# Kernel optimization log

Hardware: AMD Instinct MI355X
Metric: run time of the kernel (lower is better)

## Reference

```python
import jax, jax.numpy as jnp
import numpy as np

VOCAB = 100000
EMB = 256
HID = 512
H2 = HID // 2
TAGS = 6
START = 3
STOP = 4
NEG = -10000.0
T = 4096


def setup_inputs() -> dict:
    key = jax.random.key(0)
    ks = jax.random.split(key, 16)
    s = 0.05
    trans = jax.random.normal(ks[12], (TAGS, TAGS), dtype=jnp.float32)
    trans = trans.at[START, :].set(NEG).at[:, STOP].set(NEG)
    return {
        "sentence": jax.random.randint(ks[0], (T,), 0, VOCAB, dtype=jnp.int32),
        "emb": jax.random.normal(ks[1], (VOCAB, EMB), dtype=jnp.float32) * s,
        "w_ih_f": jax.random.normal(ks[2], (4 * H2, EMB), dtype=jnp.float32) * s,
        "w_hh_f": jax.random.normal(ks[3], (4 * H2, H2), dtype=jnp.float32) * s,
        "b_ih_f": jax.random.normal(ks[4], (4 * H2,), dtype=jnp.float32) * s,
        "b_hh_f": jax.random.normal(ks[5], (4 * H2,), dtype=jnp.float32) * s,
        "w_ih_b": jax.random.normal(ks[6], (4 * H2, EMB), dtype=jnp.float32) * s,
        "w_hh_b": jax.random.normal(ks[7], (4 * H2, H2), dtype=jnp.float32) * s,
        "b_ih_b": jax.random.normal(ks[8], (4 * H2,), dtype=jnp.float32) * s,
        "b_hh_b": jax.random.normal(ks[9], (4 * H2,), dtype=jnp.float32) * s,
        "W_out": jax.random.normal(ks[10], (TAGS, HID), dtype=jnp.float32) * s,
        "b_out": jax.random.normal(ks[11], (TAGS,), dtype=jnp.float32) * s,
        "transitions": trans,
        "h0": jax.random.normal(ks[13], (2, H2), dtype=jnp.float32),
        "c0": jax.random.normal(ks[14], (2, H2), dtype=jnp.float32),
    }


def _lstm_dir(x, h0, c0, w_ih, w_hh, b_ih, b_hh, reverse):
    # x: (T, E); PyTorch LSTM gate order i, f, g, o
    def step(carry, xt):
        h, c = carry
        z = xt @ w_ih.T + b_ih + h @ w_hh.T + b_hh
        i, f, g, o = jnp.split(z, 4)
        i = jax.nn.sigmoid(i)
        f = jax.nn.sigmoid(f)
        g = jnp.tanh(g)
        o = jax.nn.sigmoid(o)
        c = f * c + i * g
        h = o * jnp.tanh(c)
        return (h, c), h

    _, hs = jax.lax.scan(step, (h0, c0), x, reverse=reverse)
    return hs  # (T, H2), time-aligned for both directions


def reference(sentence, emb, w_ih_f, w_hh_f, b_ih_f, b_hh_f,
              w_ih_b, w_hh_b, b_ih_b, b_hh_b, W_out, b_out,
              transitions, h0, c0):
    x = emb[sentence]  # (T, E)
    hf = _lstm_dir(x, h0[0], c0[0], w_ih_f, w_hh_f, b_ih_f, b_hh_f, False)
    hb = _lstm_dir(x, h0[1], c0[1], w_ih_b, w_hh_b, b_ih_b, b_hh_b, True)
    feats = jnp.concatenate([hf, hb], axis=-1) @ W_out.T + b_out  # (T, TAGS)

    init = jnp.full((TAGS,), NEG, dtype=feats.dtype).at[START].set(0.0)

    def vstep(fv, feat):
        tmp = transitions + fv[None, :]          # (to, from)
        bp = jnp.argmax(tmp, axis=1)             # best prev tag per next tag
        fv_new = tmp[jnp.arange(TAGS), bp] + feat
        return fv_new, bp

    fv, bptrs = jax.lax.scan(vstep, init, feats)  # bptrs: (T, TAGS)
    term = fv + transitions[STOP]
    best = jnp.argmax(term)
    score = term[best]

    def btstep(tag, bp):
        return bp[tag], tag

    _, path = jax.lax.scan(btstep, best, bptrs, reverse=True)  # (T,)
    return score, path
```

## Files before the change

### kernel.cpp

```cpp
#include <hip/hip_runtime.h>
#include <stdint.h>
#include <math.h>

#define T 4096
#define NTAGS 6
#define START_TAG 3
#define STOP_TAG 4
#define NEGV -10000.0f
#define FLAG_MAGIC 0x5A000000u

__global__ __launch_bounds__(256) void k0_prep(
    const float* __restrict__ wf, const float* __restrict__ wb,
    const float* __restrict__ bif, const float* __restrict__ bhf,
    const float* __restrict__ bib, const float* __restrict__ bhb,
    float* __restrict__ wT, float* __restrict__ bias2) {
  int idx = blockIdx.x * 256 + threadIdx.x;
  int k = idx >> 11, col = idx & 2047;
  int d = col >> 10, g = col & 1023;
  const float* w = d ? wb : wf;
  wT[idx] = w[g * 256 + k];
  if (idx < 2048) bias2[idx] = d ? (bib[g] + bhb[g]) : (bif[g] + bhf[g]);
}

__global__ __launch_bounds__(256) void k1_zpre(
    const int* __restrict__ sent, const float* __restrict__ emb,
    const float* __restrict__ wT, const float* __restrict__ bias2,
    float* __restrict__ zpre) {
  int tb = blockIdx.x, cb = blockIdx.y;
  int tid = threadIdx.x;
  int col = cb * 256 + tid;
  int d = col >> 10, g = col & 1023;
  __shared__ float xs[32 * 256];
  int t0 = tb * 32;
  for (int r = 0; r < 32; r++) {
    int s = sent[t0 + r];
    xs[r * 256 + tid] = emb[(size_t)s * 256 + tid];
  }
  __syncthreads();
  float acc[32];
#pragma unroll
  for (int r = 0; r < 32; r++) acc[r] = 0.f;
  const float4* xs4 = (const float4*)xs;
  for (int kq = 0; kq < 64; kq++) {
    float w0 = wT[(4 * kq + 0) * 2048 + col];
    float w1 = wT[(4 * kq + 1) * 2048 + col];
    float w2 = wT[(4 * kq + 2) * 2048 + col];
    float w3 = wT[(4 * kq + 3) * 2048 + col];
#pragma unroll
    for (int r = 0; r < 32; r++) {
      float4 x4 = xs4[r * 64 + kq];
      acc[r] += w0 * x4.x + w1 * x4.y + w2 * x4.z + w3 * x4.w;
    }
  }
  float bb = bias2[col];
  for (int r = 0; r < 32; r++)
    zpre[((size_t)d * T + (t0 + r)) * 1024 + g] = acc[r] + bb;
}

__global__ __launch_bounds__(1024) void k2_lstm(
    const float* __restrict__ zpre,
    const float* __restrict__ whf, const float* __restrict__ whb,
    const float* __restrict__ h0, const float* __restrict__ c0,
    float* h_all, unsigned int* flags) {
  int bx = blockIdx.x;
  int d = bx >> 2, wg = bx & 3;
  const float* w_hh = d ? whb : whf;
  int tid = threadIdx.x;
  int row = tid >> 2, q = tid & 3;
  int gate = row >> 6, cl = row & 63;
  int B = wg * 64;
  int g_row = gate * 256 + B + cl;

  float4 w4[16];
  {
    const float4* wp = (const float4*)(w_hh + (size_t)g_row * 256 + q * 64);
#pragma unroll
    for (int m = 0; m < 16; m++) w4[m] = wp[m];
  }
  __shared__ float h_pad[4 * 72];
  __shared__ float z_lds[256];
  __shared__ float zin[256];
  float c = 0.f;
  if (tid < 64) c = c0[d * 256 + B + tid];
  const float* zp_d = zpre + (size_t)d * T * 1024;
  float* h_d = h_all + (size_t)d * T * 256;
  unsigned int* flg = flags + d * T * 4;

  for (int s = 0; s < T; s++) {
    int t = d ? (T - 1 - s) : s;
    float zv = 0.f;
    if (tid < 256) {
      int lg = tid >> 6, lc = tid & 63;
      zv = zp_d[(size_t)t * 1024 + lg * 256 + B + lc];
    }
    if (s == 0) {
      if (tid < 256) h_pad[(tid >> 6) * 72 + (tid & 63)] = h0[d * 256 + tid];
    } else {
      if (tid < 4) {
        unsigned int expv = FLAG_MAGIC + (unsigned)(s - 1);
        while (__hip_atomic_load(&flg[(s - 1) * 4 + tid], __ATOMIC_RELAXED,
                                 __HIP_MEMORY_SCOPE_AGENT) != expv) { }
      }
      __syncthreads();
      if (tid < 256) {
        int tprev = d ? (t + 1) : (t - 1);
        float hv = __hip_atomic_load(&h_d[(size_t)tprev * 256 + tid],
                                     __ATOMIC_RELAXED, __HIP_MEMORY_SCOPE_AGENT);
        h_pad[(tid >> 6) * 72 + (tid & 63)] = hv;
      }
    }
    if (tid < 256) zin[tid] = zv;
    __syncthreads();

    const float4* hp = (const float4*)(h_pad + q * 72);
    float acc = 0.f;
#pragma unroll
    for (int m = 0; m < 16; m++) {
      float4 h4 = hp[m];
      acc += w4[m].x * h4.x;
      acc += w4[m].y * h4.y;
      acc += w4[m].z * h4.z;
      acc += w4[m].w * h4.w;
    }
    acc += __shfl_xor(acc, 1);
    acc += __shfl_xor(acc, 2);
    if (q == 0) {
      float z = acc + zin[row];
      float a = (gate == 2) ? tanhf(z) : 1.f / (1.f + expf(-z));
      z_lds[row] = a;
    }
    __syncthreads();
    if (tid < 64) {
      float iA = z_lds[tid], fA = z_lds[64 + tid];
      float gA = z_lds[128 + tid], oA = z_lds[192 + tid];
      c = fA * c + iA * gA;
      float hv = oA * tanhf(c);
      __hip_atomic_store(&h_d[(size_t)t * 256 + B + tid], hv,
                         __ATOMIC_RELAXED, __HIP_MEMORY_SCOPE_AGENT);
    }
    __syncthreads();
    if (tid == 0) {
      __hip_atomic_store(&flg[s * 4 + wg], FLAG_MAGIC + (unsigned)s,
                         __ATOMIC_RELAXED, __HIP_MEMORY_SCOPE_AGENT);
      if (s >= 2)
        __hip_atomic_store(&flg[(s - 2) * 4 + wg], 0u,
                           __ATOMIC_RELAXED, __HIP_MEMORY_SCOPE_AGENT);
    }
  }
}

__global__ __launch_bounds__(64) void k3_feats(
    const float* __restrict__ h_all, const float* __restrict__ Wout,
    const float* __restrict__ bout, float* __restrict__ feats) {
  int t = blockIdx.x;
  int j = threadIdx.x;
  const float* hf = h_all + (size_t)t * 256;
  const float* hb = h_all + (size_t)T * 256 + (size_t)t * 256;
  float s[6];
#pragma unroll
  for (int g = 0; g < 6; g++) s[g] = 0.f;
#pragma unroll
  for (int m = 0; m < 4; m++) {
    float a = hf[j + 64 * m];
#pragma unroll
    for (int g = 0; g < 6; g++) s[g] += a * Wout[g * 512 + j + 64 * m];
  }
#pragma unroll
  for (int m = 0; m < 4; m++) {
    float b = hb[j + 64 * m];
#pragma unroll
    for (int g = 0; g < 6; g++) s[g] += b * Wout[g * 512 + 256 + j + 64 * m];
  }
#pragma unroll
  for (int g = 0; g < 6; g++) {
#pragma unroll
    for (int off = 32; off >= 1; off >>= 1) s[g] += __shfl_xor(s[g], off);
  }
  if (j < 6) feats[(size_t)t * 6 + j] = s[j] + bout[j];
}

__global__ __launch_bounds__(64) void k4_viterbi(
    const float* __restrict__ feats, const float* __restrict__ trans,
    float* __restrict__ out) {
  __shared__ unsigned char bp_lds[T * 8];
  __shared__ float fbuf[2][64 * 6];
  int lane = threadIdx.x;

  float tr[6];
#pragma unroll
  for (int f = 0; f < 6; f++) tr[f] = (lane < 6) ? trans[lane * 6 + f] : 0.f;
  float fv = (lane == START_TAG) ? 0.f : NEGV;

  for (int idx = lane; idx < 384; idx += 64) fbuf[0][idx] = feats[idx];

  for (int cch = 0; cch < 64; cch++) {
    float pf[6];
    if (cch + 1 < 64) {
#pragma unroll
      for (int m = 0; m < 6; m++)
        pf[m] = feats[(cch + 1) * 384 + lane + 64 * m];
    }
    const float* fb = fbuf[cch & 1];
    for (int j = 0; j < 64; j++) {
      int t = cch * 64 + j;
      float best = -3.4e38f;
      int bi = 0;
#pragma unroll
      for (int f = 0; f < 6; f++) {
        float v = __shfl(fv, f) + tr[f];
        if (v > best) { best = v; bi = f; }
      }
      float nfv = best + fb[j * 6 + (lane < 6 ? lane : 0)];
      if (lane < 6) {
        fv = nfv;
        bp_lds[t * 8 + lane] = (unsigned char)bi;
      }
    }
    if (cch + 1 < 64) {
#pragma unroll
      for (int m = 0; m < 6; m++)
        fbuf[(cch + 1) & 1][lane + 64 * m] = pf[m];
    }
  }

  float term = (lane < 6) ? (fv + trans[STOP_TAG * 6 + lane]) : -3.4e38f;
  float bestv = -3.4e38f;
  int bestt = 0;
#pragma unroll
  for (int f = 0; f < 6; f++) {
    float v = __shfl(term, f);
    if (v > bestv) { bestv = v; bestt = f; }
  }
  if (lane == 0) out[0] = bestv;

  unsigned int ident = 0;
#pragma unroll
  for (int i = 0; i < 6; i++) ident |= (unsigned)i << (3 * i);

  unsigned int p = ident;
  int base = lane * 64;
  for (int j2 = 0; j2 < 64; j2++) {
    const unsigned int* bw = (const unsigned int*)&bp_lds[(base + j2) * 8];
    unsigned int lo = bw[0], hi = bw[1];
    unsigned int mw = (lo & 7) | (((lo >> 8) & 7) << 3) | (((lo >> 16) & 7) << 6)
                    | (((lo >> 24) & 7) << 9) | ((hi & 7) << 12)
                    | (((hi >> 8) & 7) << 15);
    unsigned int np = 0;
#pragma unroll
    for (int i = 0; i < 6; i++) {
      unsigned int b = (mw >> (3 * i)) & 7;
      np |= ((p >> (3 * b)) & 7) << (3 * i);
    }
    p = np;
  }
  unsigned int suf = p;
#pragma unroll
  for (int off = 1; off < 64; off <<= 1) {
    unsigned int other = __shfl_down(suf, off);
    if (lane + off < 64) {
      unsigned int ns = 0;
#pragma unroll
      for (int i = 0; i < 6; i++) {
        unsigned int b = (other >> (3 * i)) & 7;
        ns |= ((suf >> (3 * b)) & 7) << (3 * i);
      }
      suf = ns;
    }
  }
  unsigned int tail = __shfl_down(suf, 1);
  if (lane == 63) tail = ident;
  unsigned int cur = tail;
  for (int j2 = 63; j2 >= 0; j2--) {
    int t = base + j2;
    out[1 + t] = (float)((cur >> (3 * bestt)) & 7);
    const unsigned int* bw = (const unsigned int*)&bp_lds[t * 8];
    unsigned int lo = bw[0], hi = bw[1];
    unsigned int mw = (lo & 7) | (((lo >> 8) & 7) << 3) | (((lo >> 16) & 7) << 6)
                    | (((lo >> 24) & 7) << 9) | ((hi & 7) << 12)
                    | (((hi >> 8) & 7) << 15);
    unsigned int nc = 0;
#pragma unroll
    for (int i = 0; i < 6; i++) {
      unsigned int b = (cur >> (3 * i)) & 7;
      nc |= ((mw >> (3 * b)) & 7) << (3 * i);
    }
    cur = nc;
  }
}

extern "C" void kernel_launch(void* const* d_in, const int* in_sizes, int n_in,
                              void* d_out, int out_size, void* d_ws, size_t ws_size,
                              hipStream_t stream) {
  const int*   sent  = (const int*)d_in[0];
  const float* emb   = (const float*)d_in[1];
  const float* wihf  = (const float*)d_in[2];
  const float* whhf  = (const float*)d_in[3];
  const float* bihf  = (const float*)d_in[4];
  const float* bhhf  = (const float*)d_in[5];
  const float* wihb  = (const float*)d_in[6];
  const float* whhb  = (const float*)d_in[7];
  const float* bihb  = (const float*)d_in[8];
  const float* bhhb  = (const float*)d_in[9];
  const float* Wout  = (const float*)d_in[10];
  const float* bout  = (const float*)d_in[11];
  const float* trans = (const float*)d_in[12];
  const float* h0    = (const float*)d_in[13];
  const float* c0    = (const float*)d_in[14];
  float* out = (float*)d_out;

  char* ws = (char*)d_ws;
  float*        zpre  = (float*)(ws + 0);
  float*        h_all = (float*)(ws + 33554432);
  float*        feats = (float*)(ws + 41943040);
  unsigned int* flags = (unsigned int*)(ws + 42041344);
  float*        wT    = (float*)(ws + 42172416);
  float*        bias2 = (float*)(ws + 44269568);

  k0_prep<<<2048, 256, 0, stream>>>(wihf, wihb, bihf, bhhf, bihb, bhhb, wT, bias2);
  dim3 g1(128, 8);
  k1_zpre<<<g1, 256, 0, stream>>>(sent, emb, wT, bias2, zpre);
  k2_lstm<<<8, 1024, 0, stream>>>(zpre, whhf, whhb, h0, c0, h_all, flags);
  k3_feats<<<4096, 64, 0, stream>>>(h_all, Wout, bout, feats);
  k4_viterbi<<<1, 64, 0, stream>>>(feats, trans, out);
}
```

Baseline: 7.641 ms.

## Replace flag-based LSTM cross-block sync with tagged-value ring polling

The recurrent LSTM kernel drops the separate per-step flag array and instead publishes each hidden value into a two-slot ring of 64-bit words holding a step tag and the value. Consumer threads poll exactly the words they need, so one barrier and a flag round-trip per step go away. Blocks shrink to 512 threads, each holding twice as many recurrent weights in registers with a shorter shuffle reduction. Gate activations switch to fast exp-based sigmoid and tanh. The risks are higher register pressure and a small precision change from the fast math.

```diff
diff --git a/kernel.cpp b/kernel.cpp
--- a/kernel.cpp
+++ b/kernel.cpp
@@ -7,7 +7,13 @@
 #define START_TAG 3
 #define STOP_TAG 4
 #define NEGV -10000.0f
-#define FLAG_MAGIC 0x5A000000u
+
+__device__ __forceinline__ float sigm_fast(float z) {
+  return 1.f / (1.f + __expf(-z));
+}
+__device__ __forceinline__ float tanh_fast(float z) {
+  return 1.f - 2.f / (1.f + __expf(2.f * z));
+}
 
 __global__ __launch_bounds__(256) void k0_prep(
     const float* __restrict__ wf, const float* __restrict__ wb,
@@ -57,94 +63,88 @@
     zpre[((size_t)d * T + (t0 + r)) * 1024 + g] = acc[r] + bb;
 }
 
-__global__ __launch_bounds__(1024) void k2_lstm(
+__global__ __launch_bounds__(512, 2) void k2_lstm(
     const float* __restrict__ zpre,
     const float* __restrict__ whf, const float* __restrict__ whb,
     const float* __restrict__ h0, const float* __restrict__ c0,
-    float* h_all, unsigned int* flags) {
+    float* h_all, unsigned long long* ring) {
   int bx = blockIdx.x;
   int d = bx >> 2, wg = bx & 3;
   const float* w_hh = d ? whb : whf;
   int tid = threadIdx.x;
-  int row = tid >> 2, q = tid & 3;
+  int row = tid >> 1, q = tid & 1;
   int gate = row >> 6, cl = row & 63;
   int B = wg * 64;
   int g_row = gate * 256 + B + cl;
 
-  float4 w4[16];
+  float4 w4[32];
   {
-    const float4* wp = (const float4*)(w_hh + (size_t)g_row * 256 + q * 64);
-#pragma unroll
-    for (int m = 0; m < 16; m++) w4[m] = wp[m];
+    const float4* wp = (const float4*)(w_hh + (size_t)g_row * 256 + q * 128);
+#pragma unroll
+    for (int m = 0; m < 32; m++) w4[m] = wp[m];
   }
   __shared__ float h_pad[4 * 72];
   __shared__ float z_lds[256];
-  __shared__ float zin[256];
   float c = 0.f;
   if (tid < 64) c = c0[d * 256 + B + tid];
   const float* zp_d = zpre + (size_t)d * T * 1024;
   float* h_d = h_all + (size_t)d * T * 256;
-  unsigned int* flg = flags + d * T * 4;
+  unsigned long long* rg = ring + (size_t)d * 2 * 256;
+
+  int chunk = tid >> 6;
+  bool is_poll = (tid < 256) && (chunk != wg);
 
   for (int s = 0; s < T; s++) {
     int t = d ? (T - 1 - s) : s;
-    float zv = 0.f;
-    if (tid < 256) {
-      int lg = tid >> 6, lc = tid & 63;
-      zv = zp_d[(size_t)t * 1024 + lg * 256 + B + lc];
-    }
+    float zself = 0.f;
+    if (q == 0) zself = zp_d[(size_t)t * 1024 + (size_t)gate * 256 + B + cl];
+
     if (s == 0) {
-      if (tid < 256) h_pad[(tid >> 6) * 72 + (tid & 63)] = h0[d * 256 + tid];
-    } else {
-      if (tid < 4) {
-        unsigned int expv = FLAG_MAGIC + (unsigned)(s - 1);
-        while (__hip_atomic_load(&flg[(s - 1) * 4 + tid], __ATOMIC_RELAXED,
-                                 __HIP_MEMORY_SCOPE_AGENT) != expv) { }
-      }
-      __syncthreads();
-      if (tid < 256) {
-        int tprev = d ? (t + 1) : (t - 1);
-        float hv = __hip_atomic_load(&h_d[(size_t)tprev * 256 + tid],
-                                     __ATOMIC_RELAXED, __HIP_MEMORY_SCOPE_AGENT);
-        h_pad[(tid >> 6) * 72 + (tid & 63)] = hv;
-      }
-    }
-    if (tid < 256) zin[tid] = zv;
+      if (tid < 256) h_pad[chunk * 72 + (tid & 63)] = h0[d * 256 + tid];
+    } else if (is_poll) {
+      unsigned exp_tag = (unsigned)(s - 1);
+      unsigned long long* addr = &rg[((s - 1) & 1) * 256 + tid];
+      unsigned long long v;
+      do {
+        v = __hip_atomic_load(addr, __ATOMIC_RELAXED, __HIP_MEMORY_SCOPE_AGENT);
+      } while ((unsigned)(v >> 32) != exp_tag);
+      union { unsigned u; float f; } cv; cv.u = (unsigned)v;
+      h_pad[chunk * 72 + (tid & 63)] = cv.f;
+    }
     __syncthreads();
 
-    const float4* hp = (const float4*)(h_pad + q * 72);
+    const float4* hp0 = (const float4*)(h_pad + (2 * q) * 72);
+    const float4* hp1 = (const float4*)(h_pad + (2 * q + 1) * 72);
     float acc = 0.f;
 #pragma unroll
     for (int m = 0; m < 16; m++) {
-      float4 h4 = hp[m];
-      acc += w4[m].x * h4.x;
-      acc += w4[m].y * h4.y;
-      acc += w4[m].z * h4.z;
-      acc += w4[m].w * h4.w;
+      float4 h4 = hp0[m];
+      acc += w4[m].x * h4.x + w4[m].y * h4.y + w4[m].z * h4.z + w4[m].w * h4.w;
+    }
+#pragma unroll
+    for (int m = 0; m < 16; m++) {
+      float4 h4 = hp1[m];
+      acc += w4[16 + m].x * h4.x + w4[16 + m].y * h4.y
+           + w4[16 + m].z * h4.z + w4[16 + m].w * h4.w;
     }
     acc += __shfl_xor(acc, 1);
-    acc += __shfl_xor(acc, 2);
     if (q == 0) {
-      float z = acc + zin[row];
-      float a = (gate == 2) ? tanhf(z) : 1.f / (1.f + expf(-z));
-      z_lds[row] = a;
+      float z = acc + zself;
+      z_lds[row] = (gate == 2) ? tanh_fast(z) : sigm_fast(z);
     }
     __syncthreads();
+
     if (tid < 64) {
       float iA = z_lds[tid], fA = z_lds[64 + tid];
       float gA = z_lds[128 + tid], oA = z_lds[192 + tid];
       c = fA * c + iA * gA;
-      float hv = oA * tanhf(c);
-      __hip_atomic_store(&h_d[(size_t)t * 256 + B + tid], hv,
+      float hv = oA * tanh_fast(c);
+      union { float f; unsigned u; } cv; cv.f = hv;
+      __hip_atomic_store(&rg[(s & 1) * 256 + B + tid],
+                         ((unsigned long long)(unsigned)s << 32) | cv.u,
                          __ATOMIC_RELAXED, __HIP_MEMORY_SCOPE_AGENT);
-    }
-    __syncthreads();
-    if (tid == 0) {
-      __hip_atomic_store(&flg[s * 4 + wg], FLAG_MAGIC + (unsigned)s,
-                         __ATOMIC_RELAXED, __HIP_MEMORY_SCOPE_AGENT);
-      if (s >= 2)
-        __hip_atomic_store(&flg[(s - 2) * 4 + wg], 0u,
-                           __ATOMIC_RELAXED, __HIP_MEMORY_SCOPE_AGENT);
+      h_pad[wg * 72 + tid] = hv;
+      h_d[(size_t)t * 256 + B + tid] = hv;
     }
   }
 }
@@ -309,17 +309,17 @@
   float* out = (float*)d_out;
 
   char* ws = (char*)d_ws;
-  float*        zpre  = (float*)(ws + 0);
-  float*        h_all = (float*)(ws + 33554432);
-  float*        feats = (float*)(ws + 41943040);
-  unsigned int* flags = (unsigned int*)(ws + 42041344);
-  float*        wT    = (float*)(ws + 42172416);
-  float*        bias2 = (float*)(ws + 44269568);
+  float*              zpre  = (float*)(ws + 0);
+  float*              h_all = (float*)(ws + 33554432);
+  float*              wT    = (float*)(ws + 41943040);
+  float*              bias2 = (float*)(ws + 44040192);
+  float*              feats = (float*)(ws + 44048384);
+  unsigned long long* ring  = (unsigned long long*)(ws + 44146688);
 
   k0_prep<<<2048, 256, 0, stream>>>(wihf, wihb, bihf, bhhf, bihb, bhhb, wT, bias2);
   dim3 g1(128, 8);
   k1_zpre<<<g1, 256, 0, stream>>>(sent, emb, wT, bias2, zpre);
-  k2_lstm<<<8, 1024, 0, stream>>>(zpre, whhf, whhb, h0, c0, h_all, flags);
+  k2_lstm<<<8, 512, 0, stream>>>(zpre, whhf, whhb, h0, c0, h_all, ring);
   k3_feats<<<4096, 64, 0, stream>>>(h_all, Wout, bout, feats);
   k4_viterbi<<<1, 64, 0, stream>>>(feats, trans, out);
 }
```

Result: slower. 8.099 ms (+6.0%).
